# Optimization experiments

Measured on AMD Instinct MI355X. Metric: run time of the kernel, lower is better.

The kernel has to match this reference:

```python
import jax, jax.numpy as jnp
import numpy as np

NUM_EXPERTS = 64
CAPACITY_FACTOR = 1.25  # capacity_factor_train, policy='argmax', is_training=True
MIN_EXPERT_CAPACITY = 4
LOSS_COEF = 0.01


def _expert_capacity(total_token_num):
    cap = float(int(total_token_num) / NUM_EXPERTS) * CAPACITY_FACTOR
    int_cap = int(cap)
    offset = 1 if cap > float(int_cap) else 0
    return max(int_cap + offset, MIN_EXPERT_CAPACITY)


def setup_inputs() -> dict:
    key = jax.random.key(0)
    k1, k2 = jax.random.split(key)
    G, S, M, E = 4, 2048, 1024, NUM_EXPERTS
    inputs = jax.random.normal(k1, (G, S, M), dtype=jnp.float32)
    gating_weight = jax.random.normal(k2, (M, E), dtype=jnp.float32) * 0.02
    return {"inputs": inputs, "gating_weight": gating_weight,
            "total_token_num": G * S}


def reference(inputs, gating_weight, total_token_num):
    E = NUM_EXPERTS
    C = _expert_capacity(total_token_num)  # static Python int

    # GSM,ME->GSE gating logits, softmax over experts
    logits = jnp.einsum('gsm,me->gse', inputs, gating_weight)
    raw_gates = jax.nn.softmax(logits, axis=-1)

    # top-1 expert
    expert_index = jnp.argmax(raw_gates, axis=2)                  # GS
    expert_mask = jax.nn.one_hot(expert_index, E, dtype=raw_gates.dtype)  # GSE

    gate_1 = jnp.sum(raw_gates * expert_mask, axis=-1)            # GS

    # exclusive cumsum over the sequence axis (position within each expert)
    position_in_expert_1 = jnp.cumsum(expert_mask, axis=1) - expert_mask  # GSE

    # aux load-balancing loss
    density_denom = 1.0 + 1e-6  # mean of ones(importance)
    density_1 = jnp.mean(expert_mask, axis=1) / density_denom      # GE
    density_1_proxy = jnp.mean(raw_gates, axis=1) / density_denom  # GE
    aux_loss = jnp.mean(density_1_proxy * density_1) * (E * E * LOSS_COEF)

    # drop tokens over capacity
    capacity = jnp.asarray(C, dtype=position_in_expert_1.dtype)
    expert_mask = expert_mask * (position_in_expert_1 < capacity).astype(expert_mask.dtype)
    pos_flat = jnp.sum(position_in_expert_1 * expert_mask, axis=-1)  # GS
    mask_1_flat = jnp.sum(expert_mask, axis=-1)                      # GS
    gate_1 = gate_1 * mask_1_flat

    # combine tensor: GSEC outer product of expert one-hot and capacity one-hot
    b = jax.nn.one_hot(pos_flat.astype(jnp.int32), C, dtype=raw_gates.dtype)   # GSC
    a = (gate_1 * mask_1_flat)[..., None] * jax.nn.one_hot(expert_index, E, dtype=raw_gates.dtype)  # GSE
    combine_tensor = jnp.einsum('gse,gsc->gsec', a, b)              # GSEC
    dispatch_mask = (combine_tensor != 0).astype(combine_tensor.dtype)

    return combine_tensor, dispatch_mask, aux_loss
```

## Files before the change

### kernel.cpp

```cpp
#include <hip/hip_runtime.h>
#include <cstddef>
#include <cstdint>

#define GG 4
#define SS 2048
#define MM 1024
#define EE 64
#define CAP 160
#define ROWQ (CAP / 4)

__global__ __launch_bounds__(256) void gating_kernel(
    const float* __restrict__ x,
    const float* __restrict__ W,
    int*   __restrict__ expert_out,
    float* __restrict__ gate_out,
    float* __restrict__ proxy)
{
    __shared__ float lds_proxy[EE];
    const int tid  = threadIdx.x;
    const int wave = tid >> 6;
    const int lane = tid & 63;

    if (tid < EE) lds_proxy[tid] = 0.0f;
    __syncthreads();

    const int t0 = blockIdx.x * 16 + wave * 4;
    const float* xr = x + (size_t)t0 * MM;

    float acc[4][4];
#pragma unroll
    for (int i = 0; i < 4; ++i)
#pragma unroll
        for (int j = 0; j < 4; ++j) acc[i][j] = 0.0f;

    for (int m = 0; m < MM; m += 4) {
        const float w0 = W[(m + 0) * EE + lane];
        const float w1 = W[(m + 1) * EE + lane];
        const float w2 = W[(m + 2) * EE + lane];
        const float w3 = W[(m + 3) * EE + lane];
#pragma unroll
        for (int i = 0; i < 4; ++i) {
            const float4 xv = *reinterpret_cast<const float4*>(xr + (size_t)i * MM + m);
            acc[i][0] = fmaf(xv.x, w0, acc[i][0]);
            acc[i][1] = fmaf(xv.y, w1, acc[i][1]);
            acc[i][2] = fmaf(xv.z, w2, acc[i][2]);
            acc[i][3] = fmaf(xv.w, w3, acc[i][3]);
        }
    }

    const int g = blockIdx.x / (SS / 16);

#pragma unroll
    for (int i = 0; i < 4; ++i) {
        double logit = ((double)acc[i][0] + (double)acc[i][1]) +
                       ((double)acc[i][2] + (double)acc[i][3]);

        double v = logit;
        int idx = lane;
        for (int off = 32; off; off >>= 1) {
            double ov = __shfl_xor(v, off);
            int    oi = __shfl_xor(idx, off);
            if (ov > v || (ov == v && oi < idx)) { v = ov; idx = oi; }
        }

        float p  = __expf((float)(logit - v));
        float ps = p;
        for (int off = 32; off; off >>= 1) ps += __shfl_xor(ps, off);
        float inv = 1.0f / ps;

        atomicAdd(&lds_proxy[lane], p * inv);

        if (lane == 0) {
            expert_out[t0 + i] = idx;
            gate_out[t0 + i]   = inv;
        }
    }

    __syncthreads();
    if (tid < EE) atomicAdd(&proxy[g * EE + tid], lds_proxy[tid]);
}

__global__ __launch_bounds__(256) void scan_kernel(
    const int* __restrict__ expert,
    int* __restrict__ pos,
    int* __restrict__ count)
{
    const int wid  = (int)((blockIdx.x * blockDim.x + threadIdx.x) >> 6);
    const int lane = threadIdx.x & 63;
    const int g = wid >> 6;
    const int e = wid & 63;
    const int* ex = expert + g * SS;

    int running = 0;
    for (int s0 = 0; s0 < SS; s0 += 64) {
        const int myex = ex[s0 + lane];
        const unsigned long long m = __ballot(myex == e);
        if (myex == e) {
            const int r = __popcll(m & ((1ull << lane) - 1ull));
            pos[g * SS + s0 + lane] = running + r;
        }
        running += __popcll(m);
    }
    if (lane == 0) count[g * EE + e] = running;
}

__global__ __launch_bounds__(256) void aux_kernel(
    const float* __restrict__ proxy,
    const int*   __restrict__ count,
    float* __restrict__ out_aux)
{
    __shared__ float red[4];
    const int i = threadIdx.x;
    const float denom = (float)SS * (1.0f + 1e-6f);
    float term = (proxy[i] / denom) * ((float)count[i] / denom);
    for (int off = 32; off; off >>= 1) term += __shfl_xor(term, off);
    if ((i & 63) == 0) red[i >> 6] = term;
    __syncthreads();
    if (i == 0) {
        float tot = (red[0] + red[1]) + (red[2] + red[3]);
        *out_aux = tot / (float)(GG * EE) * ((float)(EE * EE) * 0.01f);
    }
}

__global__ __launch_bounds__(256) void paint_kernel(
    const int*   __restrict__ expert,
    const float* __restrict__ gate,
    const int*   __restrict__ pos,
    float4* __restrict__ out)
{
    const int t   = blockIdx.x;
    const int e_t = expert[t];
    const int p   = pos[t];
    const float gv = gate[t];
    const bool kept = (p < CAP);
    const int hot_idx = e_t * ROWQ + (p >> 2);

    const size_t base = (size_t)t * (EE * ROWQ);
    const size_t N4   = (size_t)GG * SS * (EE * ROWQ);

    const float4 z = make_float4(0.f, 0.f, 0.f, 0.f);
#pragma unroll
    for (int k = 0; k < (EE * ROWQ) / 256; ++k) {
        const int idx = threadIdx.x + k * 256;
        float4 vc = z, vd = z;
        if (kept && idx == hot_idx) {
            reinterpret_cast<float*>(&vc)[p & 3] = gv;
            reinterpret_cast<float*>(&vd)[p & 3] = 1.0f;
        }
        out[base + idx]      = vc;
        out[N4 + base + idx] = vd;
    }
}

extern "C" void kernel_launch(void* const* d_in, const int* in_sizes, int n_in,
                              void* d_out, int out_size, void* d_ws, size_t ws_size,
                              hipStream_t stream) {
    const float* x = (const float*)d_in[0];
    const float* W = (const float*)d_in[1];
    float* out = (float*)d_out;

    const int tokens = GG * SS;
    const size_t N = (size_t)tokens * EE * CAP;

    float* proxy  = (float*)d_ws;
    int*   expert = (int*)(proxy + GG * EE);
    float* gate   = (float*)(expert + tokens);
    int*   pos    = (int*)(gate + tokens);
    int*   count  = (int*)(pos + tokens);

    hipMemsetAsync(proxy, 0, (size_t)(GG * EE) * sizeof(float), stream);

    gating_kernel<<<tokens / 16, 256, 0, stream>>>(x, W, expert, gate, proxy);
    scan_kernel<<<(GG * EE) / 4, 256, 0, stream>>>(expert, pos, count);
    aux_kernel<<<1, 256, 0, stream>>>(proxy, count, out + 2 * N);
    paint_kernel<<<tokens, 256, 0, stream>>>(expert, gate, pos, (float4*)out);
}
```

Measured before the change: 869.5 us.

## Use nontemporal stores for paint, fuse aux reduction into paint, drop memset and atomics

```diff
diff --git a/kernel.cpp b/kernel.cpp
--- a/kernel.cpp
+++ b/kernel.cpp
@@ -8,21 +8,22 @@
 #define EE 64
 #define CAP 160
 #define ROWQ (CAP / 4)
+#define TOKENS (GG * SS)
+#define BLK_PER_G (SS / 16)
+
+typedef float floatx4 __attribute__((ext_vector_type(4)));
 
 __global__ __launch_bounds__(256) void gating_kernel(
     const float* __restrict__ x,
     const float* __restrict__ W,
     int*   __restrict__ expert_out,
     float* __restrict__ gate_out,
-    float* __restrict__ proxy)
+    float* __restrict__ proxyp)
 {
-    __shared__ float lds_proxy[EE];
+    __shared__ float lds_p[4][EE];
     const int tid  = threadIdx.x;
     const int wave = tid >> 6;
     const int lane = tid & 63;
-
-    if (tid < EE) lds_proxy[tid] = 0.0f;
-    __syncthreads();
 
     const int t0 = blockIdx.x * 16 + wave * 4;
     const float* xr = x + (size_t)t0 * MM;
@@ -48,7 +49,7 @@
         }
     }
 
-    const int g = blockIdx.x / (SS / 16);
+    float myp = 0.0f;
 
 #pragma unroll
     for (int i = 0; i < 4; ++i) {
@@ -67,8 +68,7 @@
         float ps = p;
         for (int off = 32; off; off >>= 1) ps += __shfl_xor(ps, off);
         float inv = 1.0f / ps;
-
-        atomicAdd(&lds_proxy[lane], p * inv);
+        myp = fmaf(p, inv, myp);
 
         if (lane == 0) {
             expert_out[t0 + i] = idx;
@@ -76,8 +76,11 @@
         }
     }
 
+    lds_p[wave][lane] = myp;
     __syncthreads();
-    if (tid < EE) atomicAdd(&proxy[g * EE + tid], lds_proxy[tid]);
+    if (tid < EE)
+        proxyp[(size_t)blockIdx.x * EE + tid] =
+            (lds_p[0][tid] + lds_p[1][tid]) + (lds_p[2][tid] + lds_p[3][tid]);
 }
 
 __global__ __launch_bounds__(256) void scan_kernel(
@@ -104,30 +107,34 @@
     if (lane == 0) count[g * EE + e] = running;
 }
 
-__global__ __launch_bounds__(256) void aux_kernel(
-    const float* __restrict__ proxy,
-    const int*   __restrict__ count,
-    float* __restrict__ out_aux)
-{
-    __shared__ float red[4];
-    const int i = threadIdx.x;
-    const float denom = (float)SS * (1.0f + 1e-6f);
-    float term = (proxy[i] / denom) * ((float)count[i] / denom);
-    for (int off = 32; off; off >>= 1) term += __shfl_xor(term, off);
-    if ((i & 63) == 0) red[i >> 6] = term;
-    __syncthreads();
-    if (i == 0) {
-        float tot = (red[0] + red[1]) + (red[2] + red[3]);
-        *out_aux = tot / (float)(GG * EE) * ((float)(EE * EE) * 0.01f);
-    }
-}
-
 __global__ __launch_bounds__(256) void paint_kernel(
     const int*   __restrict__ expert,
     const float* __restrict__ gate,
     const int*   __restrict__ pos,
-    float4* __restrict__ out)
+    const float* __restrict__ proxyp,
+    const int*   __restrict__ count,
+    floatx4* __restrict__ out,
+    float*  __restrict__ out_aux)
 {
+    if (blockIdx.x == TOKENS) {
+        __shared__ float red[4];
+        const int i = threadIdx.x;
+        const int g = i >> 6, e = i & 63;
+        float s = 0.0f;
+        for (int j = 0; j < BLK_PER_G; ++j)
+            s += proxyp[(size_t)(g * BLK_PER_G + j) * EE + e];
+        const float denom = (float)SS * (1.0f + 1e-6f);
+        float term = (s / denom) * ((float)count[i] / denom);
+        for (int off = 32; off; off >>= 1) term += __shfl_xor(term, off);
+        if ((i & 63) == 0) red[i >> 6] = term;
+        __syncthreads();
+        if (i == 0) {
+            float tot = (red[0] + red[1]) + (red[2] + red[3]);
+            *out_aux = tot / (float)(GG * EE) * ((float)(EE * EE) * 0.01f);
+        }
+        return;
+    }
+
     const int t   = blockIdx.x;
     const int e_t = expert[t];
     const int p   = pos[t];
@@ -136,19 +143,19 @@
     const int hot_idx = e_t * ROWQ + (p >> 2);
 
     const size_t base = (size_t)t * (EE * ROWQ);
-    const size_t N4   = (size_t)GG * SS * (EE * ROWQ);
+    const size_t N4   = (size_t)TOKENS * (EE * ROWQ);
 
-    const float4 z = make_float4(0.f, 0.f, 0.f, 0.f);
+    const floatx4 z = (floatx4)(0.0f);
 #pragma unroll
     for (int k = 0; k < (EE * ROWQ) / 256; ++k) {
         const int idx = threadIdx.x + k * 256;
-        float4 vc = z, vd = z;
+        floatx4 vc = z, vd = z;
         if (kept && idx == hot_idx) {
-            reinterpret_cast<float*>(&vc)[p & 3] = gv;
-            reinterpret_cast<float*>(&vd)[p & 3] = 1.0f;
+            vc[p & 3] = gv;
+            vd[p & 3] = 1.0f;
         }
-        out[base + idx]      = vc;
-        out[N4 + base + idx] = vd;
+        __builtin_nontemporal_store(vc, &out[base + idx]);
+        __builtin_nontemporal_store(vd, &out[N4 + base + idx]);
     }
 }
 
@@ -159,19 +166,16 @@
     const float* W = (const float*)d_in[1];
     float* out = (float*)d_out;
 
-    const int tokens = GG * SS;
-    const size_t N = (size_t)tokens * EE * CAP;
+    const size_t N = (size_t)TOKENS * EE * CAP;
 
-    float* proxy  = (float*)d_ws;
-    int*   expert = (int*)(proxy + GG * EE);
-    float* gate   = (float*)(expert + tokens);
-    int*   pos    = (int*)(gate + tokens);
-    int*   count  = (int*)(pos + tokens);
+    float* proxyp = (float*)d_ws;
+    int*   expert = (int*)(proxyp + (TOKENS / 16) * EE);
+    float* gate   = (float*)(expert + TOKENS);
+    int*   pos    = (int*)(gate + TOKENS);
+    int*   count  = (int*)(pos + TOKENS);
 
-    hipMemsetAsync(proxy, 0, (size_t)(GG * EE) * sizeof(float), stream);
-
-    gating_kernel<<<tokens / 16, 256, 0, stream>>>(x, W, expert, gate, proxy);
+    gating_kernel<<<TOKENS / 16, 256, 0, stream>>>(x, W, expert, gate, proxyp);
     scan_kernel<<<(GG * EE) / 4, 256, 0, stream>>>(expert, pos, count);
-    aux_kernel<<<1, 256, 0, stream>>>(proxy, count, out + 2 * N);
-    paint_kernel<<<tokens, 256, 0, stream>>>(expert, gate, pos, (float4*)out);
+    paint_kernel<<<TOKENS + 1, 256, 0, stream>>>(expert, gate, pos, proxyp, count,
+                                                 (floatx4*)out, out + 2 * N);
 }
```

Measured after the change: 853.5 us. About the same (-1.8%).
